# Optimization experiments

Measured on AMD Instinct MI355X. Metric: run time of the kernel, lower is better.

The kernel has to match this reference:

```python
import jax, jax.numpy as jnp
import numpy as np
import math

D_MODEL = 1024
NUM_HEADS = 16
D_K = D_MODEL // NUM_HEADS
MAX_LEN = 2048
B, S = 2, 1024


def setup_inputs() -> dict:
    key = jax.random.key(0)
    ks = jax.random.split(key, 10)
    lin_scale = 1.0 / math.sqrt(D_MODEL)
    # torch Linear: weight (out, in), y = x @ W.T + b
    Wq = jax.random.uniform(ks[0], (D_MODEL, D_MODEL), jnp.float32, -lin_scale, lin_scale)
    Wk = jax.random.uniform(ks[1], (D_MODEL, D_MODEL), jnp.float32, -lin_scale, lin_scale)
    Wv = jax.random.uniform(ks[2], (D_MODEL, D_MODEL), jnp.float32, -lin_scale, lin_scale)
    Wo = jax.random.uniform(ks[3], (D_MODEL, D_MODEL), jnp.float32, -lin_scale, lin_scale)
    bq = jnp.zeros((D_MODEL,), jnp.float32)
    bk = jnp.zeros((D_MODEL,), jnp.float32)
    bv = jnp.zeros((D_MODEL,), jnp.float32)
    bo = jnp.zeros((D_MODEL,), jnp.float32)
    # xavier_uniform for Er (max_len, d_k)
    er_bound = math.sqrt(6.0 / (MAX_LEN + D_K))
    Er = jax.random.uniform(ks[4], (MAX_LEN, D_K), jnp.float32, -er_bound, er_bound)
    x = jax.random.normal(ks[5], (B, S, D_MODEL), jnp.float32)
    return {"x": x, "Wq": Wq, "bq": bq, "Wk": Wk, "bk": bk,
            "Wv": Wv, "bv": bv, "Wo": Wo, "bo": bo, "Er": Er}


def reference(x, Wq, bq, Wk, bk, Wv, bv, Wo, bo, Er):
    Bsz, Slen, Dm = x.shape
    H, dk = NUM_HEADS, D_K

    def proj(W, b):
        y = jnp.einsum('bsd,ed->bse', x, W) + b
        return y.reshape(Bsz, Slen, H, dk).transpose(0, 2, 1, 3)  # (B,H,S,dk)

    Q = proj(Wq, bq)
    K = proj(Wk, bk)
    V = proj(Wv, bv)

    # content-content scores
    AC = jnp.einsum('bhid,bhjd->bhij', Q, K)  # (B,H,S,S)

    # relative position embeddings for distances S-1 .. -(S-1)
    rel_pos = jnp.arange(Slen - 1, -Slen, -1)  # (2S-1,)
    idx = rel_pos + (Slen - 1)                 # map to 0..2S-2 (requires 2S-1 <= max_len)
    Er_emb = Er[idx]                           # (2S-1, dk)
    BD_full = jnp.einsum('bhid,md->bhim', Q, Er_emb)  # (B,H,S,2S-1)

    # relative shift: final[i,j] = BD_full[i, S-1 - i + j] (column for distance i-j)
    i_idx = jnp.arange(Slen)[:, None]                  # (S,1)
    m_idx = (Slen - 1) - i_idx + jnp.arange(Slen)[None, :]  # (S,S)
    BD = BD_full[:, :, i_idx, m_idx]                   # (B,H,S,S)

    scores = (AC + BD) / math.sqrt(dk)
    attn = jax.nn.softmax(scores, axis=-1)  # dropout is identity at eval
    out = jnp.einsum('bhij,bhjd->bhid', attn, V)       # (B,H,S,dk)
    out = out.transpose(0, 2, 1, 3).reshape(Bsz, Slen, Dm)
    return jnp.einsum('bsd,ed->bse', out, Wo) + bo
```

## Files before the change

### kernel.cpp

```cpp
#include <hip/hip_runtime.h>
#include <hip/hip_bf16.h>
#include <math.h>

#define D_MODEL 1024
#define NUM_HEADS 16
#define D_K 64
#define SEQ 1024
#define BATCH 2

typedef __hip_bfloat16 bf16;
typedef __bf16 bf16x8 __attribute__((ext_vector_type(8)));
typedef __bf16 bf16x4 __attribute__((ext_vector_type(4)));
typedef float floatx4 __attribute__((ext_vector_type(4)));

__device__ __forceinline__ floatx4 mfma16(bf16x8 a, bf16x8 b, floatx4 c) {
    return __builtin_amdgcn_mfma_f32_16x16x32_bf16(a, b, c, 0, 0, 0);
}

__global__ void detect_dtype_kernel(const void* __restrict__ x, int* __restrict__ flag) {
    __shared__ int cnt[256];
    const float* xf = (const float*)x;
    const int tid = threadIdx.x;
    int sane = 0;
    for (int i = tid; i < 4096; i += 256) {
        float v = xf[i];
        float a = fabsf(v);
        if (v == 0.0f || (a > 1e-8f && a < 1e8f)) sane++;
    }
    cnt[tid] = sane;
    __syncthreads();
    for (int s = 128; s > 0; s >>= 1) {
        if (tid < s) cnt[tid] += cnt[tid + s];
        __syncthreads();
    }
    if (tid == 0) flag[0] = (cnt[0] > 3686) ? 1 : 0;
}

struct ConvSrcs { const void* p[10]; };

__global__ __launch_bounds__(256) void convert_all_kernel(ConvSrcs srcs,
                                                          bf16* __restrict__ dstbase,
                                                          const int* __restrict__ flag) {
    const long long e = ((long long)blockIdx.x * 256 + threadIdx.x) * 8;
    int seg; long long base;
    if      (e < 2097152LL) { seg = 0; base = 0; }
    else if (e < 3145728LL) { seg = 1; base = 2097152LL; }
    else if (e < 4194304LL) { seg = 2; base = 3145728LL; }
    else if (e < 5242880LL) { seg = 3; base = 4194304LL; }
    else if (e < 6291456LL) { seg = 4; base = 5242880LL; }
    else if (e < 6292480LL) { seg = 5; base = 6291456LL; }
    else if (e < 6293504LL) { seg = 6; base = 6292480LL; }
    else if (e < 6294528LL) { seg = 7; base = 6293504LL; }
    else if (e < 6295552LL) { seg = 8; base = 6294528LL; }
    else                    { seg = 9; base = 6295552LL; }
    const long long local = e - base;
    __bf16 tmp[8];
    if (*flag) {
        const float* s = (const float*)srcs.p[seg] + local;
#pragma unroll
        for (int t = 0; t < 8; ++t) tmp[t] = (__bf16)s[t];
        *(bf16x8*)(void*)(dstbase + e) = *(const bf16x8*)tmp;
    } else {
        *(bf16x8*)(void*)(dstbase + e) =
            *(const bf16x8*)(const void*)((const bf16*)srcs.p[seg] + local);
    }
}

__global__ __launch_bounds__(256) void gemm_qkv_kernel(const bf16* __restrict__ x,
        const bf16* __restrict__ Wq, const bf16* __restrict__ Wk, const bf16* __restrict__ Wv,
        const bf16* __restrict__ bq, const bf16* __restrict__ bk, const bf16* __restrict__ bv,
        bf16* __restrict__ Qb, bf16* __restrict__ Kb, bf16* __restrict__ Vb) {
    const int wsel = blockIdx.x >> 3;
    const int n0 = (blockIdx.x & 7) * 128;
    const int m0 = blockIdx.y * 128;
    const bf16* W    = (wsel == 0) ? Wq : ((wsel == 1) ? Wk : Wv);
    const bf16* bias = (wsel == 0) ? bq : ((wsel == 1) ? bk : bv);
    bf16* Cb         = (wsel == 0) ? Qb : ((wsel == 1) ? Kb : Vb);

    __shared__ __bf16 As[128][72];
    __shared__ __bf16 Bs[128][72];
    const int tid = threadIdx.x;
    const int wave = tid >> 6, lane = tid & 63, quad = lane >> 4, l16 = lane & 15;
    const int wr = (wave >> 1) * 64, wc = (wave & 1) * 64;
    const int srow = tid >> 1, scg = (tid & 1) * 32;

    floatx4 acc[4][4];
#pragma unroll
    for (int r = 0; r < 4; ++r)
#pragma unroll
        for (int c = 0; c < 4; ++c) acc[r][c] = (floatx4)0.f;

    for (int k0 = 0; k0 < 1024; k0 += 64) {
        const bf16* ag = x + (size_t)(m0 + srow) * 1024 + k0 + scg;
        const bf16* bg = W + (size_t)(n0 + srow) * 1024 + k0 + scg;
        bf16x8 av[4], bv[4];
#pragma unroll
        for (int c = 0; c < 4; ++c) {
            av[c] = *(const bf16x8*)(const void*)(ag + c * 8);
            bv[c] = *(const bf16x8*)(const void*)(bg + c * 8);
        }
        __syncthreads();
#pragma unroll
        for (int c = 0; c < 4; ++c) {
            *(bf16x8*)&As[srow][scg + c * 8] = av[c];
            *(bf16x8*)&Bs[srow][scg + c * 8] = bv[c];
        }
        __syncthreads();
#pragma unroll
        for (int kk = 0; kk < 2; ++kk) {
            bf16x8 af[4], bfr[4];
#pragma unroll
            for (int r = 0; r < 4; ++r)
                af[r] = *(const bf16x8*)&As[wr + r * 16 + l16][kk * 32 + quad * 8];
#pragma unroll
            for (int c = 0; c < 4; ++c)
                bfr[c] = *(const bf16x8*)&Bs[wc + c * 16 + l16][kk * 32 + quad * 8];
#pragma unroll
            for (int r = 0; r < 4; ++r)
#pragma unroll
                for (int c = 0; c < 4; ++c)
                    acc[r][c] = mfma16(af[r], bfr[c], acc[r][c]);
        }
    }
#pragma unroll
    for (int c = 0; c < 4; ++c) {
        const int col = n0 + wc + c * 16 + l16;
        const float bvl = (float)bias[col];
#pragma unroll
        for (int r = 0; r < 4; ++r)
#pragma unroll
            for (int v = 0; v < 4; ++v) {
                const int row = m0 + wr + r * 16 + quad * 4 + v;
                Cb[(size_t)row * 1024 + col] = (bf16)(acc[r][c][v] + bvl);
            }
    }
}

__global__ __launch_bounds__(256) void gemm_out_kernel(const bf16* __restrict__ A,
        const bf16* __restrict__ W, const bf16* __restrict__ bias,
        void* __restrict__ C, const int* __restrict__ flag) {
    const int n0 = blockIdx.x * 64;
    const int m0 = blockIdx.y * 128;
    __shared__ __bf16 As[128][72];
    __shared__ __bf16 Bs[64][72];
    const int tid = threadIdx.x;
    const int wave = tid >> 6, lane = tid & 63, quad = lane >> 4, l16 = lane & 15;
    const int wr = (wave >> 1) * 64, wc = (wave & 1) * 32;
    const int arow = tid >> 1, acg = (tid & 1) * 32;
    const int brow = tid >> 2, bcg = (tid & 3) * 16;

    floatx4 acc[4][2];
#pragma unroll
    for (int r = 0; r < 4; ++r)
#pragma unroll
        for (int c = 0; c < 2; ++c) acc[r][c] = (floatx4)0.f;

    for (int k0 = 0; k0 < 1024; k0 += 64) {
        const bf16* ag = A + (size_t)(m0 + arow) * 1024 + k0 + acg;
        const bf16* bg = W + (size_t)(n0 + brow) * 1024 + k0 + bcg;
        bf16x8 av[4], bv[2];
#pragma unroll
        for (int c = 0; c < 4; ++c) av[c] = *(const bf16x8*)(const void*)(ag + c * 8);
#pragma unroll
        for (int c = 0; c < 2; ++c) bv[c] = *(const bf16x8*)(const void*)(bg + c * 8);
        __syncthreads();
#pragma unroll
        for (int c = 0; c < 4; ++c) *(bf16x8*)&As[arow][acg + c * 8] = av[c];
#pragma unroll
        for (int c = 0; c < 2; ++c) *(bf16x8*)&Bs[brow][bcg + c * 8] = bv[c];
        __syncthreads();
#pragma unroll
        for (int kk = 0; kk < 2; ++kk) {
            bf16x8 af[4], bfr[2];
#pragma unroll
            for (int r = 0; r < 4; ++r)
                af[r] = *(const bf16x8*)&As[wr + r * 16 + l16][kk * 32 + quad * 8];
#pragma unroll
            for (int c = 0; c < 2; ++c)
                bfr[c] = *(const bf16x8*)&Bs[wc + c * 16 + l16][kk * 32 + quad * 8];
#pragma unroll
            for (int r = 0; r < 4; ++r)
#pragma unroll
                for (int c = 0; c < 2; ++c)
                    acc[r][c] = mfma16(af[r], bfr[c], acc[r][c]);
        }
    }
#pragma unroll
    for (int c = 0; c < 2; ++c) {
        const int col = n0 + wc + c * 16 + l16;
        const float bvl = (float)bias[col];
#pragma unroll
        for (int r = 0; r < 4; ++r)
#pragma unroll
            for (int v = 0; v < 4; ++v) {
                const int row = m0 + wr + r * 16 + quad * 4 + v;
                const float val = acc[r][c][v] + bvl;
                const size_t idx = (size_t)row * 1024 + col;
                if (*flag) ((float*)C)[idx] = val;
                else       ((bf16*)C)[idx] = (bf16)val;
            }
    }
}

__global__ __launch_bounds__(256) void transpose_v_kernel(const bf16* __restrict__ V,
                                                          bf16* __restrict__ Vt) {
    __shared__ __bf16 Ls[64][72];
    const int s0 = blockIdx.x * 64;
    const int h = blockIdx.y, b = blockIdx.z;
    const int tid = threadIdx.x;
    {
        const int r = tid >> 2, cg = (tid & 3) * 16;
        const bf16* g = V + ((size_t)(b * SEQ + s0 + r)) * D_MODEL + h * 64 + cg;
        *(bf16x8*)&Ls[r][cg]     = *(const bf16x8*)(const void*)g;
        *(bf16x8*)&Ls[r][cg + 8] = *(const bf16x8*)(const void*)(g + 8);
    }
    __syncthreads();
    {
        const int d = tid >> 2, cs = (tid & 3) * 16;
        __bf16 tmp[16];
#pragma unroll
        for (int t = 0; t < 16; ++t) tmp[t] = Ls[cs + t][d];
        bf16* g = Vt + ((size_t)((b * NUM_HEADS + h) * 64 + d)) * SEQ + s0 + cs;
        *(bf16x8*)(void*)g       = *(const bf16x8*)tmp;
        *(bf16x8*)(void*)(g + 8) = *(const bf16x8*)(tmp + 8);
    }
}

__global__ __launch_bounds__(128) void attn_mfma_kernel(const bf16* __restrict__ Q,
                                                        const bf16* __restrict__ Kc,
                                                        const bf16* __restrict__ Vt,
                                                        const bf16* __restrict__ Er,
                                                        bf16* __restrict__ O) {
    const int i0 = blockIdx.x * 64;
    const int h = blockIdx.y, b = blockIdx.z;
    const int tid = threadIdx.x;
    const int wave = tid >> 6, lane = tid & 63, quad = lane >> 4, l16 = lane & 15;

    __shared__ __bf16 Qs[64][72];
    __shared__ __bf16 Ks[64][72];
    __shared__ __bf16 Vs[64][72];
    __shared__ __bf16 Ers[128][72];
    __bf16* scr = &Ers[0][0] + wave * 3456;

    const size_t qk_base = (size_t)b * SEQ * D_MODEL + h * 64;

    {
        const int r = tid >> 1, cg = (tid & 1) * 32;
        const bf16* g = Q + qk_base + (size_t)(i0 + r) * D_MODEL + cg;
#pragma unroll
        for (int c = 0; c < 32; c += 8)
            *(bf16x8*)&Qs[r][cg + c] = *(const bf16x8*)(const void*)(g + c);
    }
    __syncthreads();
    bf16x8 aq[2][2];
#pragma unroll
    for (int half = 0; half < 2; ++half)
#pragma unroll
        for (int kk = 0; kk < 2; ++kk)
            aq[half][kk] = *(const bf16x8*)&Qs[wave * 32 + half * 16 + l16][kk * 32 + quad * 8];

    floatx4 oacc[4][2];
#pragma unroll
    for (int ct = 0; ct < 4; ++ct)
#pragma unroll
        for (int half = 0; half < 2; ++half) oacc[ct][half] = (floatx4)0.f;
    float m_i[2][4], l_i[2][4];
#pragma unroll
    for (int half = 0; half < 2; ++half)
#pragma unroll
        for (int v = 0; v < 4; ++v) { m_i[half][v] = -1e30f; l_i[half][v] = 0.f; }

    const int eb = 960 + i0;
    const bf16* Kg = Kc + qk_base;
    const bf16* Vtg = Vt + (size_t)((b * NUM_HEADS + h) * 64) * SEQ;

    for (int j0 = 0; j0 < SEQ; j0 += 64) {
        __syncthreads();
        {
            const int r = tid >> 1, cg = (tid & 1) * 32;
            const bf16* kg = Kg + (size_t)(j0 + r) * D_MODEL + cg;
            const bf16* vg = Vtg + (size_t)r * SEQ + j0 + cg;
#pragma unroll
            for (int c = 0; c < 32; c += 8) {
                *(bf16x8*)&Ks[r][cg + c] = *(const bf16x8*)(const void*)(kg + c);
                *(bf16x8*)&Vs[r][cg + c] = *(const bf16x8*)(const void*)(vg + c);
            }
            const bf16* eg = Er + (size_t)(eb - j0 + tid) * 64;
#pragma unroll
            for (int c = 0; c < 64; c += 8)
                *(bf16x8*)&Ers[tid][c] = *(const bf16x8*)(const void*)(eg + c);
        }
        __syncthreads();

        floatx4 sfrag[4][2];
#pragma unroll
        for (int ct = 0; ct < 4; ++ct) {
            bf16x8 bk0 = *(const bf16x8*)&Ks[ct * 16 + l16][quad * 8];
            bf16x8 bk1 = *(const bf16x8*)&Ks[ct * 16 + l16][32 + quad * 8];
#pragma unroll
            for (int half = 0; half < 2; ++half) {
                floatx4 s = (floatx4)0.f;
                s = mfma16(aq[half][0], bk0, s);
                s = mfma16(aq[half][1], bk1, s);
                sfrag[ct][half] = s;
            }
        }
        floatx4 tacc[6][2];
#pragma unroll
        for (int ct = 0; ct < 6; ++ct) {
            bf16x8 be0 = *(const bf16x8*)&Ers[wave * 32 + ct * 16 + l16][quad * 8];
            bf16x8 be1 = *(const bf16x8*)&Ers[wave * 32 + ct * 16 + l16][32 + quad * 8];
#pragma unroll
            for (int half = 0; half < 2; ++half) {
                floatx4 t = (floatx4)0.f;
                t = mfma16(aq[half][0], be0, t);
                t = mfma16(aq[half][1], be1, t);
                tacc[ct][half] = t;
            }
        }
        __syncthreads();

#pragma unroll
        for (int ct = 0; ct < 6; ++ct)
#pragma unroll
            for (int half = 0; half < 2; ++half) {
                bf16x4 tv;
#pragma unroll
                for (int v = 0; v < 4; ++v) tv[v] = (__bf16)tacc[ct][half][v];
                *(bf16x4*)(void*)(scr + (ct * 16 + l16) * 36 + half * 16 + quad * 4) = tv;
            }
#pragma unroll
        for (int ct = 0; ct < 4; ++ct)
#pragma unroll
            for (int half = 0; half < 2; ++half)
#pragma unroll
                for (int v = 0; v < 4; ++v) {
                    const int rl = half * 16 + quad * 4 + v;
                    const int cl = 63 + rl - (ct * 16 + l16);
                    sfrag[ct][half][v] =
                        (sfrag[ct][half][v] + (float)scr[cl * 36 + rl]) * 0.125f;
                }
        float alpha[2][4];
#pragma unroll
        for (int half = 0; half < 2; ++half) {
#pragma unroll
            for (int v = 0; v < 4; ++v) {
                float mx = fmaxf(fmaxf(sfrag[0][half][v], sfrag[1][half][v]),
                                 fmaxf(sfrag[2][half][v], sfrag[3][half][v]));
#pragma unroll
                for (int off = 1; off < 16; off <<= 1)
                    mx = fmaxf(mx, __shfl_xor(mx, off, 64));
                const float mnew = fmaxf(m_i[half][v], mx);
                alpha[half][v] = __expf(m_i[half][v] - mnew);
                m_i[half][v] = mnew;
            }
            float rs[4] = {0.f, 0.f, 0.f, 0.f};
#pragma unroll
            for (int ct = 0; ct < 4; ++ct)
#pragma unroll
                for (int v = 0; v < 4; ++v) {
                    const float p = __expf(sfrag[ct][half][v] - m_i[half][v]);
                    sfrag[ct][half][v] = p;
                    rs[v] += p;
                }
#pragma unroll
            for (int v = 0; v < 4; ++v) {
                float s = rs[v];
#pragma unroll
                for (int off = 1; off < 16; off <<= 1)
                    s += __shfl_xor(s, off, 64);
                l_i[half][v] = l_i[half][v] * alpha[half][v] + s;
            }
        }
#pragma unroll
        for (int ct = 0; ct < 4; ++ct)
#pragma unroll
            for (int half = 0; half < 2; ++half)
#pragma unroll
                for (int v = 0; v < 4; ++v)
                    scr[(half * 16 + quad * 4 + v) * 72 + ct * 16 + l16] =
                        (__bf16)sfrag[ct][half][v];
#pragma unroll
        for (int ct = 0; ct < 4; ++ct)
#pragma unroll
            for (int half = 0; half < 2; ++half)
#pragma unroll
                for (int v = 0; v < 4; ++v) oacc[ct][half][v] *= alpha[half][v];
        bf16x8 ap[2][2];
#pragma unroll
        for (int half = 0; half < 2; ++half)
#pragma unroll
            for (int kk = 0; kk < 2; ++kk)
                ap[half][kk] =
                    *(const bf16x8*)(const void*)(scr + (half * 16 + l16) * 72 + kk * 32 + quad * 8);
#pragma unroll
        for (int ct = 0; ct < 4; ++ct) {
            bf16x8 bv0 = *(const bf16x8*)&Vs[ct * 16 + l16][quad * 8];
            bf16x8 bv1 = *(const bf16x8*)&Vs[ct * 16 + l16][32 + quad * 8];
#pragma unroll
            for (int half = 0; half < 2; ++half) {
                oacc[ct][half] = mfma16(ap[half][0], bv0, oacc[ct][half]);
                oacc[ct][half] = mfma16(ap[half][1], bv1, oacc[ct][half]);
            }
        }
    }
#pragma unroll
    for (int ct = 0; ct < 4; ++ct)
#pragma unroll
        for (int half = 0; half < 2; ++half)
#pragma unroll
            for (int v = 0; v < 4; ++v) {
                const int row = i0 + wave * 32 + half * 16 + quad * 4 + v;
                const int col = h * 64 + ct * 16 + l16;
                O[((size_t)b * SEQ + row) * D_MODEL + col] =
                    (bf16)(oacc[ct][half][v] / l_i[half][v]);
            }
}

extern "C" void kernel_launch(void* const* d_in, const int* in_sizes, int n_in,
                              void* d_out, int out_size, void* d_ws, size_t ws_size,
                              hipStream_t stream) {
    const int M = BATCH * SEQ;
    const size_t E_X = (size_t)M * D_MODEL;
    const size_t E_CANON = 6426624;

    char* ws = (char*)d_ws;
    int* flag = (int*)ws;
    bf16* canon = (bf16*)(ws + 16);
    bf16* xc  = canon;
    bf16* Wqc = canon + 2097152;
    bf16* Wkc = canon + 3145728;
    bf16* Wvc = canon + 4194304;
    bf16* Woc = canon + 5242880;
    bf16* bqc = canon + 6291456;
    bf16* bkc = canon + 6292480;
    bf16* bvc = canon + 6293504;
    bf16* boc = canon + 6294528;
    bf16* Erc = canon + 6295552;
    bf16* p = canon + E_CANON;
    bf16* Qb = p;  p += E_X;
    bf16* Kb = p;  p += E_X;
    bf16* Vb = p;  p += E_X;
    bf16* Vt = p;  p += E_X;
    bf16* Ob = p;  p += E_X;

    detect_dtype_kernel<<<1, 256, 0, stream>>>(d_in[0], flag);

    ConvSrcs cs;
    cs.p[0] = d_in[0]; cs.p[1] = d_in[1]; cs.p[2] = d_in[3]; cs.p[3] = d_in[5];
    cs.p[4] = d_in[7]; cs.p[5] = d_in[2]; cs.p[6] = d_in[4]; cs.p[7] = d_in[6];
    cs.p[8] = d_in[8]; cs.p[9] = d_in[9];
    convert_all_kernel<<<3138, 256, 0, stream>>>(cs, canon, flag);

    gemm_qkv_kernel<<<dim3(24, 16), 256, 0, stream>>>(xc, Wqc, Wkc, Wvc,
                                                      bqc, bkc, bvc, Qb, Kb, Vb);

    transpose_v_kernel<<<dim3(16, NUM_HEADS, BATCH), 256, 0, stream>>>(Vb, Vt);

    attn_mfma_kernel<<<dim3(SEQ / 64, NUM_HEADS, BATCH), 128, 0, stream>>>(Qb, Kb, Vt, Erc, Ob);

    gemm_out_kernel<<<dim3(16, 16), 256, 0, stream>>>(Ob, Woc, boc, d_out, flag);
}
```

Baseline: 204.3 us.

## Fuse V transpose into QKV GEMM, split attention KV range, add combine kernel

The QKV GEMM now uses 128x64 tiles with more blocks and writes V directly in transposed per-head layout, so the separate transpose kernel goes away. Attention now uses 128-query blocks of 4 waves and splits the key range into two halves across blocks. It computes the row sum with an extra MFMA column of ones instead of shuffles, and writes partial outputs plus max and sum stats. A new combine kernel merges the two halves, and the output GEMM uses smaller 64x64 tiles for more blocks. The aim is better occupancy and fewer launches, at the cost of extra partial-output traffic and one extra kernel.

New measurement: 195.5 us. -4.3%, faster.

```diff
diff --git a/kernel.cpp b/kernel.cpp
--- a/kernel.cpp
+++ b/kernel.cpp
@@ -69,78 +69,13 @@
 __global__ __launch_bounds__(256) void gemm_qkv_kernel(const bf16* __restrict__ x,
         const bf16* __restrict__ Wq, const bf16* __restrict__ Wk, const bf16* __restrict__ Wv,
         const bf16* __restrict__ bq, const bf16* __restrict__ bk, const bf16* __restrict__ bv,
-        bf16* __restrict__ Qb, bf16* __restrict__ Kb, bf16* __restrict__ Vb) {
-    const int wsel = blockIdx.x >> 3;
-    const int n0 = (blockIdx.x & 7) * 128;
+        bf16* __restrict__ Qb, bf16* __restrict__ Kb, bf16* __restrict__ Vt) {
+    const int wsel = blockIdx.x >> 4;
+    const int n0 = (blockIdx.x & 15) * 64;
     const int m0 = blockIdx.y * 128;
     const bf16* W    = (wsel == 0) ? Wq : ((wsel == 1) ? Wk : Wv);
     const bf16* bias = (wsel == 0) ? bq : ((wsel == 1) ? bk : bv);
-    bf16* Cb         = (wsel == 0) ? Qb : ((wsel == 1) ? Kb : Vb);
-
-    __shared__ __bf16 As[128][72];
-    __shared__ __bf16 Bs[128][72];
-    const int tid = threadIdx.x;
-    const int wave = tid >> 6, lane = tid & 63, quad = lane >> 4, l16 = lane & 15;
-    const int wr = (wave >> 1) * 64, wc = (wave & 1) * 64;
-    const int srow = tid >> 1, scg = (tid & 1) * 32;
-
-    floatx4 acc[4][4];
-#pragma unroll
-    for (int r = 0; r < 4; ++r)
-#pragma unroll
-        for (int c = 0; c < 4; ++c) acc[r][c] = (floatx4)0.f;
-
-    for (int k0 = 0; k0 < 1024; k0 += 64) {
-        const bf16* ag = x + (size_t)(m0 + srow) * 1024 + k0 + scg;
-        const bf16* bg = W + (size_t)(n0 + srow) * 1024 + k0 + scg;
-        bf16x8 av[4], bv[4];
-#pragma unroll
-        for (int c = 0; c < 4; ++c) {
-            av[c] = *(const bf16x8*)(const void*)(ag + c * 8);
-            bv[c] = *(const bf16x8*)(const void*)(bg + c * 8);
-        }
-        __syncthreads();
-#pragma unroll
-        for (int c = 0; c < 4; ++c) {
-            *(bf16x8*)&As[srow][scg + c * 8] = av[c];
-            *(bf16x8*)&Bs[srow][scg + c * 8] = bv[c];
-        }
-        __syncthreads();
-#pragma unroll
-        for (int kk = 0; kk < 2; ++kk) {
-            bf16x8 af[4], bfr[4];
-#pragma unroll
-            for (int r = 0; r < 4; ++r)
-                af[r] = *(const bf16x8*)&As[wr + r * 16 + l16][kk * 32 + quad * 8];
-#pragma unroll
-            for (int c = 0; c < 4; ++c)
-                bfr[c] = *(const bf16x8*)&Bs[wc + c * 16 + l16][kk * 32 + quad * 8];
-#pragma unroll
-            for (int r = 0; r < 4; ++r)
-#pragma unroll
-                for (int c = 0; c < 4; ++c)
-                    acc[r][c] = mfma16(af[r], bfr[c], acc[r][c]);
-        }
-    }
-#pragma unroll
-    for (int c = 0; c < 4; ++c) {
-        const int col = n0 + wc + c * 16 + l16;
-        const float bvl = (float)bias[col];
-#pragma unroll
-        for (int r = 0; r < 4; ++r)
-#pragma unroll
-            for (int v = 0; v < 4; ++v) {
-                const int row = m0 + wr + r * 16 + quad * 4 + v;
-                Cb[(size_t)row * 1024 + col] = (bf16)(acc[r][c][v] + bvl);
-            }
-    }
-}
-
-__global__ __launch_bounds__(256) void gemm_out_kernel(const bf16* __restrict__ A,
-        const bf16* __restrict__ W, const bf16* __restrict__ bias,
-        void* __restrict__ C, const int* __restrict__ flag) {
-    const int n0 = blockIdx.x * 64;
-    const int m0 = blockIdx.y * 128;
+
     __shared__ __bf16 As[128][72];
     __shared__ __bf16 Bs[64][72];
     const int tid = threadIdx.x;
@@ -156,18 +91,18 @@
         for (int c = 0; c < 2; ++c) acc[r][c] = (floatx4)0.f;
 
     for (int k0 = 0; k0 < 1024; k0 += 64) {
-        const bf16* ag = A + (size_t)(m0 + arow) * 1024 + k0 + acg;
+        const bf16* ag = x + (size_t)(m0 + arow) * 1024 + k0 + acg;
         const bf16* bg = W + (size_t)(n0 + brow) * 1024 + k0 + bcg;
-        bf16x8 av[4], bv[2];
+        bf16x8 av[4], bv2[2];
 #pragma unroll
         for (int c = 0; c < 4; ++c) av[c] = *(const bf16x8*)(const void*)(ag + c * 8);
 #pragma unroll
-        for (int c = 0; c < 2; ++c) bv[c] = *(const bf16x8*)(const void*)(bg + c * 8);
+        for (int c = 0; c < 2; ++c) bv2[c] = *(const bf16x8*)(const void*)(bg + c * 8);
         __syncthreads();
 #pragma unroll
         for (int c = 0; c < 4; ++c) *(bf16x8*)&As[arow][acg + c * 8] = av[c];
 #pragma unroll
-        for (int c = 0; c < 2; ++c) *(bf16x8*)&Bs[brow][bcg + c * 8] = bv[c];
+        for (int c = 0; c < 2; ++c) *(bf16x8*)&Bs[brow][bcg + c * 8] = bv2[c];
         __syncthreads();
 #pragma unroll
         for (int kk = 0; kk < 2; ++kk) {
@@ -180,6 +115,300 @@
                 bfr[c] = *(const bf16x8*)&Bs[wc + c * 16 + l16][kk * 32 + quad * 8];
 #pragma unroll
             for (int r = 0; r < 4; ++r)
+#pragma unroll
+                for (int c = 0; c < 2; ++c)
+                    acc[r][c] = mfma16(af[r], bfr[c], acc[r][c]);
+        }
+    }
+
+    if (wsel < 2) {
+        bf16* Cb = (wsel == 0) ? Qb : Kb;
+#pragma unroll
+        for (int c = 0; c < 2; ++c) {
+            const int col = n0 + wc + c * 16 + l16;
+            const float bvl = (float)bias[col];
+#pragma unroll
+            for (int r = 0; r < 4; ++r)
+#pragma unroll
+                for (int v = 0; v < 4; ++v) {
+                    const int row = m0 + wr + r * 16 + quad * 4 + v;
+                    Cb[(size_t)row * 1024 + col] = (bf16)(acc[r][c][v] + bvl);
+                }
+        }
+    } else {
+        __bf16* Ls = &As[0][0];
+        __syncthreads();
+#pragma unroll
+        for (int c = 0; c < 2; ++c) {
+            const int col = wc + c * 16 + l16;
+            const float bvl = (float)bias[n0 + col];
+#pragma unroll
+            for (int r = 0; r < 4; ++r)
+#pragma unroll
+                for (int v = 0; v < 4; ++v) {
+                    const int row = wr + r * 16 + quad * 4 + v;
+                    Ls[col * 132 + row] = (__bf16)(acc[r][c][v] + bvl);
+                }
+        }
+        __syncthreads();
+        const int b = m0 >> 10, s0 = m0 & 1023, h = n0 >> 6;
+        const int d = tid >> 2, sg = (tid & 3) * 32;
+        bf16* g = Vt + ((size_t)((b * NUM_HEADS + h) * 64 + d)) * SEQ + s0 + sg;
+#pragma unroll
+        for (int c = 0; c < 32; c += 8)
+            *(bf16x8*)(void*)(g + c) = *(const bf16x8*)&Ls[d * 132 + sg + c];
+    }
+}
+
+__global__ __launch_bounds__(256) void attn_mfma_kernel(const bf16* __restrict__ Q,
+                                                        const bf16* __restrict__ Kc,
+                                                        const bf16* __restrict__ Vt,
+                                                        const bf16* __restrict__ Er,
+                                                        bf16* __restrict__ Opart,
+                                                        float* __restrict__ Ml) {
+    const int i0 = blockIdx.x * 128;
+    const int h = blockIdx.y;
+    const int b = blockIdx.z >> 1, jsel = blockIdx.z & 1;
+    const int tid = threadIdx.x;
+    const int wave = tid >> 6, lane = tid & 63, quad = lane >> 4, l16 = lane & 15;
+
+    __shared__ __bf16 Ks[64][72];
+    __shared__ __bf16 Vs[80][72];
+    __shared__ __bf16 Ers[192][72];
+    __shared__ __bf16 scr_all[4][3264];
+    __bf16* scr = &scr_all[wave][0];
+    __bf16* Qs = &scr_all[0][0];
+
+    for (int e = tid; e < 16 * 72; e += 256) {
+        const int r = e / 72, c = e - r * 72;
+        Vs[64 + r][c] = (r == 0) ? (__bf16)1.0f : (__bf16)0.0f;
+    }
+    {
+        const int r = tid >> 1, cg = (tid & 1) * 32;
+        const bf16* g = Q + ((size_t)(b * SEQ + i0 + r)) * D_MODEL + h * 64 + cg;
+#pragma unroll
+        for (int c = 0; c < 32; c += 8)
+            *(bf16x8*)(void*)(Qs + r * 72 + cg + c) = *(const bf16x8*)(const void*)(g + c);
+    }
+    __syncthreads();
+    bf16x8 aq[2][2];
+#pragma unroll
+    for (int half = 0; half < 2; ++half)
+#pragma unroll
+        for (int kk = 0; kk < 2; ++kk)
+            aq[half][kk] = *(const bf16x8*)(const void*)(
+                Qs + (wave * 32 + half * 16 + l16) * 72 + kk * 32 + quad * 8);
+
+    floatx4 oacc[5][2];
+#pragma unroll
+    for (int ct = 0; ct < 5; ++ct)
+#pragma unroll
+        for (int half = 0; half < 2; ++half) oacc[ct][half] = (floatx4)0.f;
+    float m_i[2][4];
+#pragma unroll
+    for (int half = 0; half < 2; ++half)
+#pragma unroll
+        for (int v = 0; v < 4; ++v) m_i[half][v] = -1e30f;
+
+    const int eb = 960 + i0;
+    const bf16* Kg = Kc + (size_t)b * SEQ * D_MODEL + h * 64;
+    const bf16* Vtg = Vt + (size_t)((b * NUM_HEADS + h) * 64) * SEQ;
+
+    const int jbeg = jsel * 512, jend = jbeg + 512;
+    for (int j0 = jbeg; j0 < jend; j0 += 64) {
+        __syncthreads();
+        {
+            const int r4 = tid >> 2, c4 = (tid & 3) * 16;
+            const bf16* kg = Kg + (size_t)(j0 + r4) * D_MODEL + c4;
+            const bf16* vg = Vtg + (size_t)r4 * SEQ + j0 + c4;
+            *(bf16x8*)&Ks[r4][c4]     = *(const bf16x8*)(const void*)kg;
+            *(bf16x8*)&Ks[r4][c4 + 8] = *(const bf16x8*)(const void*)(kg + 8);
+            *(bf16x8*)&Vs[r4][c4]     = *(const bf16x8*)(const void*)vg;
+            *(bf16x8*)&Vs[r4][c4 + 8] = *(const bf16x8*)(const void*)(vg + 8);
+            for (int s = tid; s < 384; s += 256) {
+                const int er = s >> 1, ecg = (s & 1) * 32;
+                const bf16* eg = Er + (size_t)(eb - j0 + er) * 64 + ecg;
+#pragma unroll
+                for (int c = 0; c < 32; c += 8)
+                    *(bf16x8*)&Ers[er][ecg + c] = *(const bf16x8*)(const void*)(eg + c);
+            }
+        }
+        __syncthreads();
+
+        floatx4 sfrag[4][2];
+#pragma unroll
+        for (int ct = 0; ct < 4; ++ct) {
+            bf16x8 bk0 = *(const bf16x8*)&Ks[ct * 16 + l16][quad * 8];
+            bf16x8 bk1 = *(const bf16x8*)&Ks[ct * 16 + l16][32 + quad * 8];
+#pragma unroll
+            for (int half = 0; half < 2; ++half) {
+                floatx4 s = (floatx4)0.f;
+                s = mfma16(aq[half][0], bk0, s);
+                s = mfma16(aq[half][1], bk1, s);
+                sfrag[ct][half] = s;
+            }
+        }
+#pragma unroll
+        for (int ct = 0; ct < 6; ++ct) {
+            bf16x8 be0 = *(const bf16x8*)&Ers[wave * 32 + ct * 16 + l16][quad * 8];
+            bf16x8 be1 = *(const bf16x8*)&Ers[wave * 32 + ct * 16 + l16][32 + quad * 8];
+#pragma unroll
+            for (int half = 0; half < 2; ++half) {
+                floatx4 t = (floatx4)0.f;
+                t = mfma16(aq[half][0], be0, t);
+                t = mfma16(aq[half][1], be1, t);
+                bf16x4 tv;
+#pragma unroll
+                for (int v = 0; v < 4; ++v) tv[v] = (__bf16)t[v];
+                *(bf16x4*)(void*)(scr + (ct * 16 + l16) * 34 + half * 16 + quad * 4) = tv;
+            }
+        }
+#pragma unroll
+        for (int ct = 0; ct < 4; ++ct)
+#pragma unroll
+            for (int half = 0; half < 2; ++half)
+#pragma unroll
+                for (int v = 0; v < 4; ++v) {
+                    const int rl = half * 16 + quad * 4 + v;
+                    const int cl = 63 + rl - (ct * 16 + l16);
+                    sfrag[ct][half][v] =
+                        (sfrag[ct][half][v] + (float)scr[cl * 34 + rl]) * 0.125f;
+                }
+        float alpha[2][4];
+#pragma unroll
+        for (int half = 0; half < 2; ++half)
+#pragma unroll
+            for (int v = 0; v < 4; ++v) {
+                float mx = fmaxf(fmaxf(sfrag[0][half][v], sfrag[1][half][v]),
+                                 fmaxf(sfrag[2][half][v], sfrag[3][half][v]));
+#pragma unroll
+                for (int off = 1; off < 16; off <<= 1)
+                    mx = fmaxf(mx, __shfl_xor(mx, off, 64));
+                const float mnew = fmaxf(m_i[half][v], mx);
+                alpha[half][v] = __expf(m_i[half][v] - mnew);
+                m_i[half][v] = mnew;
+            }
+#pragma unroll
+        for (int ct = 0; ct < 4; ++ct)
+#pragma unroll
+            for (int half = 0; half < 2; ++half)
+#pragma unroll
+                for (int v = 0; v < 4; ++v) {
+                    const float p = __expf(sfrag[ct][half][v] - m_i[half][v]);
+                    scr[(half * 16 + quad * 4 + v) * 72 + ct * 16 + l16] = (__bf16)p;
+                }
+#pragma unroll
+        for (int ct = 0; ct < 5; ++ct)
+#pragma unroll
+            for (int half = 0; half < 2; ++half)
+#pragma unroll
+                for (int v = 0; v < 4; ++v) oacc[ct][half][v] *= alpha[half][v];
+        bf16x8 ap[2][2];
+#pragma unroll
+        for (int half = 0; half < 2; ++half)
+#pragma unroll
+            for (int kk = 0; kk < 2; ++kk)
+                ap[half][kk] = *(const bf16x8*)(const void*)(
+                    scr + (half * 16 + l16) * 72 + kk * 32 + quad * 8);
+#pragma unroll
+        for (int ct = 0; ct < 5; ++ct) {
+            bf16x8 bv0 = *(const bf16x8*)&Vs[ct * 16 + l16][quad * 8];
+            bf16x8 bv1 = *(const bf16x8*)&Vs[ct * 16 + l16][32 + quad * 8];
+#pragma unroll
+            for (int half = 0; half < 2; ++half) {
+                oacc[ct][half] = mfma16(ap[half][0], bv0, oacc[ct][half]);
+                oacc[ct][half] = mfma16(ap[half][1], bv1, oacc[ct][half]);
+            }
+        }
+    }
+
+    bf16* Op = Opart + (size_t)jsel * 2097152;
+#pragma unroll
+    for (int ct = 0; ct < 4; ++ct)
+#pragma unroll
+        for (int half = 0; half < 2; ++half)
+#pragma unroll
+            for (int v = 0; v < 4; ++v) {
+                const int row = i0 + wave * 32 + half * 16 + quad * 4 + v;
+                const int col = h * 64 + ct * 16 + l16;
+                Op[((size_t)(b * SEQ + row)) * D_MODEL + col] = (bf16)oacc[ct][half][v];
+            }
+    if (l16 == 0) {
+        const int base = ((jsel * 2 + b) * 16 + h) * 1024;
+#pragma unroll
+        for (int half = 0; half < 2; ++half)
+#pragma unroll
+            for (int v = 0; v < 4; ++v) {
+                const int ig = i0 + wave * 32 + half * 16 + quad * 4 + v;
+                Ml[base + ig] = m_i[half][v];
+                Ml[65536 + base + ig] = oacc[4][half][v];
+            }
+    }
+}
+
+__global__ __launch_bounds__(256) void combine_kernel(const bf16* __restrict__ Opart,
+                                                      const float* __restrict__ Ml,
+                                                      bf16* __restrict__ Ob) {
+    const int e = (blockIdx.x * 256 + threadIdx.x) * 4;
+    const int row = e >> 10, col = e & 1023;
+    const int b = row >> 10, i = row & 1023, h = col >> 6;
+    const int mb = b * 16384 + h * 1024 + i;
+    const float m1 = Ml[mb], m2 = Ml[32768 + mb];
+    const float l1 = Ml[65536 + mb], l2 = Ml[65536 + 32768 + mb];
+    const float mm = fmaxf(m1, m2);
+    const float e1 = __expf(m1 - mm), e2 = __expf(m2 - mm);
+    const float inv = 1.0f / (e1 * l1 + e2 * l2);
+    bf16x4 o1 = *(const bf16x4*)(const void*)(Opart + e);
+    bf16x4 o2 = *(const bf16x4*)(const void*)(Opart + 2097152 + e);
+    bf16x4 o;
+#pragma unroll
+    for (int v = 0; v < 4; ++v)
+        o[v] = (__bf16)((e1 * (float)o1[v] + e2 * (float)o2[v]) * inv);
+    *(bf16x4*)(void*)(Ob + e) = o;
+}
+
+__global__ __launch_bounds__(256) void gemm_out_kernel(const bf16* __restrict__ A,
+        const bf16* __restrict__ W, const bf16* __restrict__ bias,
+        void* __restrict__ C, const int* __restrict__ flag) {
+    const int n0 = blockIdx.x * 64;
+    const int m0 = blockIdx.y * 64;
+    __shared__ __bf16 As[64][72];
+    __shared__ __bf16 Bs[64][72];
+    const int tid = threadIdx.x;
+    const int wave = tid >> 6, lane = tid & 63, quad = lane >> 4, l16 = lane & 15;
+    const int wr = (wave >> 1) * 32, wc = (wave & 1) * 32;
+    const int srow = tid >> 2, scg = (tid & 3) * 16;
+
+    floatx4 acc[2][2];
+#pragma unroll
+    for (int r = 0; r < 2; ++r)
+#pragma unroll
+        for (int c = 0; c < 2; ++c) acc[r][c] = (floatx4)0.f;
+
+    for (int k0 = 0; k0 < 1024; k0 += 64) {
+        const bf16* ag = A + (size_t)(m0 + srow) * 1024 + k0 + scg;
+        const bf16* bg = W + (size_t)(n0 + srow) * 1024 + k0 + scg;
+        bf16x8 av0 = *(const bf16x8*)(const void*)ag;
+        bf16x8 av1 = *(const bf16x8*)(const void*)(ag + 8);
+        bf16x8 bv0 = *(const bf16x8*)(const void*)bg;
+        bf16x8 bv1 = *(const bf16x8*)(const void*)(bg + 8);
+        __syncthreads();
+        *(bf16x8*)&As[srow][scg]     = av0;
+        *(bf16x8*)&As[srow][scg + 8] = av1;
+        *(bf16x8*)&Bs[srow][scg]     = bv0;
+        *(bf16x8*)&Bs[srow][scg + 8] = bv1;
+        __syncthreads();
+#pragma unroll
+        for (int kk = 0; kk < 2; ++kk) {
+            bf16x8 af[2], bfr[2];
+#pragma unroll
+            for (int r = 0; r < 2; ++r)
+                af[r] = *(const bf16x8*)&As[wr + r * 16 + l16][kk * 32 + quad * 8];
+#pragma unroll
+            for (int c = 0; c < 2; ++c)
+                bfr[c] = *(const bf16x8*)&Bs[wc + c * 16 + l16][kk * 32 + quad * 8];
+#pragma unroll
+            for (int r = 0; r < 2; ++r)
 #pragma unroll
                 for (int c = 0; c < 2; ++c)
                     acc[r][c] = mfma16(af[r], bfr[c], acc[r][c]);
@@ -190,7 +419,7 @@
         const int col = n0 + wc + c * 16 + l16;
         const float bvl = (float)bias[col];
 #pragma unroll
-        for (int r = 0; r < 4; ++r)
+        for (int r = 0; r < 2; ++r)
 #pragma unroll
             for (int v = 0; v < 4; ++v) {
                 const int row = m0 + wr + r * 16 + quad * 4 + v;
@@ -202,226 +431,10 @@
     }
 }
 
-__global__ __launch_bounds__(256) void transpose_v_kernel(const bf16* __restrict__ V,
-                                                          bf16* __restrict__ Vt) {
-    __shared__ __bf16 Ls[64][72];
-    const int s0 = blockIdx.x * 64;
-    const int h = blockIdx.y, b = blockIdx.z;
-    const int tid = threadIdx.x;
-    {
-        const int r = tid >> 2, cg = (tid & 3) * 16;
-        const bf16* g = V + ((size_t)(b * SEQ + s0 + r)) * D_MODEL + h * 64 + cg;
-        *(bf16x8*)&Ls[r][cg]     = *(const bf16x8*)(const void*)g;
-        *(bf16x8*)&Ls[r][cg + 8] = *(const bf16x8*)(const void*)(g + 8);
-    }
-    __syncthreads();
-    {
-        const int d = tid >> 2, cs = (tid & 3) * 16;
-        __bf16 tmp[16];
-#pragma unroll
-        for (int t = 0; t < 16; ++t) tmp[t] = Ls[cs + t][d];
-        bf16* g = Vt + ((size_t)((b * NUM_HEADS + h) * 64 + d)) * SEQ + s0 + cs;
-        *(bf16x8*)(void*)g       = *(const bf16x8*)tmp;
-        *(bf16x8*)(void*)(g + 8) = *(const bf16x8*)(tmp + 8);
-    }
-}
-
-__global__ __launch_bounds__(128) void attn_mfma_kernel(const bf16* __restrict__ Q,
-                                                        const bf16* __restrict__ Kc,
-                                                        const bf16* __restrict__ Vt,
-                                                        const bf16* __restrict__ Er,
-                                                        bf16* __restrict__ O) {
-    const int i0 = blockIdx.x * 64;
-    const int h = blockIdx.y, b = blockIdx.z;
-    const int tid = threadIdx.x;
-    const int wave = tid >> 6, lane = tid & 63, quad = lane >> 4, l16 = lane & 15;
-
-    __shared__ __bf16 Qs[64][72];
-    __shared__ __bf16 Ks[64][72];
-    __shared__ __bf16 Vs[64][72];
-    __shared__ __bf16 Ers[128][72];
-    __bf16* scr = &Ers[0][0] + wave * 3456;
-
-    const size_t qk_base = (size_t)b * SEQ * D_MODEL + h * 64;
-
-    {
-        const int r = tid >> 1, cg = (tid & 1) * 32;
-        const bf16* g = Q + qk_base + (size_t)(i0 + r) * D_MODEL + cg;
-#pragma unroll
-        for (int c = 0; c < 32; c += 8)
-            *(bf16x8*)&Qs[r][cg + c] = *(const bf16x8*)(const void*)(g + c);
-    }
-    __syncthreads();
-    bf16x8 aq[2][2];
-#pragma unroll
-    for (int half = 0; half < 2; ++half)
-#pragma unroll
-        for (int kk = 0; kk < 2; ++kk)
-            aq[half][kk] = *(const bf16x8*)&Qs[wave * 32 + half * 16 + l16][kk * 32 + quad * 8];
-
-    floatx4 oacc[4][2];
-#pragma unroll
-    for (int ct = 0; ct < 4; ++ct)
-#pragma unroll
-        for (int half = 0; half < 2; ++half) oacc[ct][half] = (floatx4)0.f;
-    float m_i[2][4], l_i[2][4];
-#pragma unroll
-    for (int half = 0; half < 2; ++half)
-#pragma unroll
-        for (int v = 0; v < 4; ++v) { m_i[half][v] = -1e30f; l_i[half][v] = 0.f; }
-
-    const int eb = 960 + i0;
-    const bf16* Kg = Kc + qk_base;
-    const bf16* Vtg = Vt + (size_t)((b * NUM_HEADS + h) * 64) * SEQ;
-
-    for (int j0 = 0; j0 < SEQ; j0 += 64) {
-        __syncthreads();
-        {
-            const int r = tid >> 1, cg = (tid & 1) * 32;
-            const bf16* kg = Kg + (size_t)(j0 + r) * D_MODEL + cg;
-            const bf16* vg = Vtg + (size_t)r * SEQ + j0 + cg;
-#pragma unroll
-            for (int c = 0; c < 32; c += 8) {
-                *(bf16x8*)&Ks[r][cg + c] = *(const bf16x8*)(const void*)(kg + c);
-                *(bf16x8*)&Vs[r][cg + c] = *(const bf16x8*)(const void*)(vg + c);
-            }
-            const bf16* eg = Er + (size_t)(eb - j0 + tid) * 64;
-#pragma unroll
-            for (int c = 0; c < 64; c += 8)
-                *(bf16x8*)&Ers[tid][c] = *(const bf16x8*)(const void*)(eg + c);
-        }
-        __syncthreads();
-
-        floatx4 sfrag[4][2];
-#pragma unroll
-        for (int ct = 0; ct < 4; ++ct) {
-            bf16x8 bk0 = *(const bf16x8*)&Ks[ct * 16 + l16][quad * 8];
-            bf16x8 bk1 = *(const bf16x8*)&Ks[ct * 16 + l16][32 + quad * 8];
-#pragma unroll
-            for (int half = 0; half < 2; ++half) {
-                floatx4 s = (floatx4)0.f;
-                s = mfma16(aq[half][0], bk0, s);
-                s = mfma16(aq[half][1], bk1, s);
-                sfrag[ct][half] = s;
-            }
-        }
-        floatx4 tacc[6][2];
-#pragma unroll
-        for (int ct = 0; ct < 6; ++ct) {
-            bf16x8 be0 = *(const bf16x8*)&Ers[wave * 32 + ct * 16 + l16][quad * 8];
-            bf16x8 be1 = *(const bf16x8*)&Ers[wave * 32 + ct * 16 + l16][32 + quad * 8];
-#pragma unroll
-            for (int half = 0; half < 2; ++half) {
-                floatx4 t = (floatx4)0.f;
-                t = mfma16(aq[half][0], be0, t);
-                t = mfma16(aq[half][1], be1, t);
-                tacc[ct][half] = t;
-            }
-        }
-        __syncthreads();
-
-#pragma unroll
-        for (int ct = 0; ct < 6; ++ct)
-#pragma unroll
-            for (int half = 0; half < 2; ++half) {
-                bf16x4 tv;
-#pragma unroll
-                for (int v = 0; v < 4; ++v) tv[v] = (__bf16)tacc[ct][half][v];
-                *(bf16x4*)(void*)(scr + (ct * 16 + l16) * 36 + half * 16 + quad * 4) = tv;
-            }
-#pragma unroll
-        for (int ct = 0; ct < 4; ++ct)
-#pragma unroll
-            for (int half = 0; half < 2; ++half)
-#pragma unroll
-                for (int v = 0; v < 4; ++v) {
-                    const int rl = half * 16 + quad * 4 + v;
-                    const int cl = 63 + rl - (ct * 16 + l16);
-                    sfrag[ct][half][v] =
-                        (sfrag[ct][half][v] + (float)scr[cl * 36 + rl]) * 0.125f;
-                }
-        float alpha[2][4];
-#pragma unroll
-        for (int half = 0; half < 2; ++half) {
-#pragma unroll
-            for (int v = 0; v < 4; ++v) {
-                float mx = fmaxf(fmaxf(sfrag[0][half][v], sfrag[1][half][v]),
-                                 fmaxf(sfrag[2][half][v], sfrag[3][half][v]));
-#pragma unroll
-                for (int off = 1; off < 16; off <<= 1)
-                    mx = fmaxf(mx, __shfl_xor(mx, off, 64));
-                const float mnew = fmaxf(m_i[half][v], mx);
-                alpha[half][v] = __expf(m_i[half][v] - mnew);
-                m_i[half][v] = mnew;
-            }
-            float rs[4] = {0.f, 0.f, 0.f, 0.f};
-#pragma unroll
-            for (int ct = 0; ct < 4; ++ct)
-#pragma unroll
-                for (int v = 0; v < 4; ++v) {
-                    const float p = __expf(sfrag[ct][half][v] - m_i[half][v]);
-                    sfrag[ct][half][v] = p;
-                    rs[v] += p;
-                }
-#pragma unroll
-            for (int v = 0; v < 4; ++v) {
-                float s = rs[v];
-#pragma unroll
-                for (int off = 1; off < 16; off <<= 1)
-                    s += __shfl_xor(s, off, 64);
-                l_i[half][v] = l_i[half][v] * alpha[half][v] + s;
-            }
-        }
-#pragma unroll
-        for (int ct = 0; ct < 4; ++ct)
-#pragma unroll
-            for (int half = 0; half < 2; ++half)
-#pragma unroll
-                for (int v = 0; v < 4; ++v)
-                    scr[(half * 16 + quad * 4 + v) * 72 + ct * 16 + l16] =
-                        (__bf16)sfrag[ct][half][v];
-#pragma unroll
-        for (int ct = 0; ct < 4; ++ct)
-#pragma unroll
-            for (int half = 0; half < 2; ++half)
-#pragma unroll
-                for (int v = 0; v < 4; ++v) oacc[ct][half][v] *= alpha[half][v];
-        bf16x8 ap[2][2];
-#pragma unroll
-        for (int half = 0; half < 2; ++half)
-#pragma unroll
-            for (int kk = 0; kk < 2; ++kk)
-                ap[half][kk] =
-                    *(const bf16x8*)(const void*)(scr + (half * 16 + l16) * 72 + kk * 32 + quad * 8);
-#pragma unroll
-        for (int ct = 0; ct < 4; ++ct) {
-            bf16x8 bv0 = *(const bf16x8*)&Vs[ct * 16 + l16][quad * 8];
-            bf16x8 bv1 = *(const bf16x8*)&Vs[ct * 16 + l16][32 + quad * 8];
-#pragma unroll
-            for (int half = 0; half < 2; ++half) {
-                oacc[ct][half] = mfma16(ap[half][0], bv0, oacc[ct][half]);
-                oacc[ct][half] = mfma16(ap[half][1], bv1, oacc[ct][half]);
-            }
-        }
-    }
-#pragma unroll
-    for (int ct = 0; ct < 4; ++ct)
-#pragma unroll
-        for (int half = 0; half < 2; ++half)
-#pragma unroll
-            for (int v = 0; v < 4; ++v) {
-                const int row = i0 + wave * 32 + half * 16 + quad * 4 + v;
-                const int col = h * 64 + ct * 16 + l16;
-                O[((size_t)b * SEQ + row) * D_MODEL + col] =
-                    (bf16)(oacc[ct][half][v] / l_i[half][v]);
-            }
-}
-
 extern "C" void kernel_launch(void* const* d_in, const int* in_sizes, int n_in,
                               void* d_out, int out_size, void* d_ws, size_t ws_size,
                               hipStream_t stream) {
-    const int M = BATCH * SEQ;
-    const size_t E_X = (size_t)M * D_MODEL;
+    const size_t E_X = 2097152;
     const size_t E_CANON = 6426624;
 
     char* ws = (char*)d_ws;
@@ -438,11 +451,11 @@
     bf16* boc = canon + 6294528;
     bf16* Erc = canon + 6295552;
     bf16* p = canon + E_CANON;
-    bf16* Qb = p;  p += E_X;
-    bf16* Kb = p;  p += E_X;
-    bf16* Vb = p;  p += E_X;
-    bf16* Vt = p;  p += E_X;
-    bf16* Ob = p;  p += E_X;
+    bf16* Qb    = p;  p += E_X;
+    bf16* Kb    = p;  p += E_X;
+    bf16* Vt    = p;  p += E_X;
+    bf16* Opart = p;  p += 2 * E_X;
+    float* Ml   = (float*)p;
 
     detect_dtype_kernel<<<1, 256, 0, stream>>>(d_in[0], flag);
 
@@ -452,12 +465,12 @@
     cs.p[8] = d_in[8]; cs.p[9] = d_in[9];
     convert_all_kernel<<<3138, 256, 0, stream>>>(cs, canon, flag);
 
-    gemm_qkv_kernel<<<dim3(24, 16), 256, 0, stream>>>(xc, Wqc, Wkc, Wvc,
-                                                      bqc, bkc, bvc, Qb, Kb, Vb);
-
-    transpose_v_kernel<<<dim3(16, NUM_HEADS, BATCH), 256, 0, stream>>>(Vb, Vt);
-
-    attn_mfma_kernel<<<dim3(SEQ / 64, NUM_HEADS, BATCH), 128, 0, stream>>>(Qb, Kb, Vt, Erc, Ob);
-
-    gemm_out_kernel<<<dim3(16, 16), 256, 0, stream>>>(Ob, Woc, boc, d_out, flag);
-}
+    gemm_qkv_kernel<<<dim3(48, 16), 256, 0, stream>>>(xc, Wqc, Wkc, Wvc,
+                                                      bqc, bkc, bvc, Qb, Kb, Vt);
+
+    attn_mfma_kernel<<<dim3(8, 16, 4), 256, 0, stream>>>(Qb, Kb, Vt, Erc, Opart, Ml);
+
+    combine_kernel<<<2048, 256, 0, stream>>>(Opart, Ml, Qb);
+
+    gemm_out_kernel<<<dim3(16, 32), 256, 0, stream>>>(Qb, Woc, boc, d_out, flag);
+}
```
